# Performance work log

Hardware: AMD Instinct MI355X
Metric: run time of the kernel (lower is better)

The kernel has to match this reference:

```python
import jax, jax.numpy as jnp
import numpy as np

NUM_HEADS = 8
NUM_POINTS = 4


def setup_inputs() -> dict:
    key = jax.random.key(0)
    ks = jax.random.split(key, 10)
    B, H, W, D = 8, 64, 64, 256
    N = H * W
    nh, P = NUM_HEADS, NUM_POINTS

    def xavier(k, shape):
        fan_in, fan_out = shape[0], shape[1]
        lim = float(np.sqrt(6.0 / (fan_in + fan_out)))
        return jax.random.uniform(k, shape, jnp.float32, -lim, lim)

    x = jax.random.normal(ks[0], (B, N, D), jnp.float32)
    qkv_w = xavier(ks[1], (D, 3 * D))
    qkv_b = jnp.zeros((3 * D,), jnp.float32)
    # offset network is zero-init in the module; use small random weights so the
    # deformable sampling is actually exercised (offsets nonzero).
    off_w = jax.random.normal(ks[2], (D, nh * P * 2), jnp.float32) * 0.01
    off_b = jnp.zeros((nh * P * 2,), jnp.float32)
    attw_w = xavier(ks[3], (D, nh * P))
    attw_b = jnp.zeros((nh * P,), jnp.float32)
    proj_w = xavier(ks[4], (D, D))
    proj_b = jnp.zeros((D,), jnp.float32)
    return {
        "x": x, "qkv_w": qkv_w, "qkv_b": qkv_b,
        "off_w": off_w, "off_b": off_b,
        "attw_w": attw_w, "attw_b": attw_b,
        "proj_w": proj_w, "proj_b": proj_b,
        "H": 64, "W": 64,
    }


def _deformable_forward(x, qkv_w, qkv_b, off_w, off_b, attw_w, attw_b, proj_w, proj_b, H, W):
    B, N, D = x.shape
    nh, P = NUM_HEADS, NUM_POINTS
    hd = D // nh

    qkv = x @ qkv_w + qkv_b                      # [B,N,3D] (q,k computed but unused, as in the original)
    v = qkv[..., 2 * D:].reshape(B, N, nh, hd)   # [B,N,nh,hd]

    offsets = jnp.tanh((x @ off_w + off_b).reshape(B, N, nh, P, 2)) * 2.0

    ys, xs = jnp.meshgrid(jnp.arange(H, dtype=x.dtype), jnp.arange(W, dtype=x.dtype), indexing="ij")
    ref = jnp.stack([xs, ys], axis=-1).reshape(N, 2)          # [N,2] (x,y) pixel coords
    loc = ref[None, :, None, None, :] + offsets               # [B,N,nh,P,2] pixel coords
    # (module normalizes to [-1,1] then grid_sample align_corners=True un-normalizes
    #  back to exactly these pixel coordinates, so we sample at `loc` directly)

    # value as flat spatial map per head: [B,nh,hd,N], n = y*W + x
    vf = v.transpose(0, 2, 3, 1).reshape(B, nh, hd, N)

    gx, gy = loc[..., 0], loc[..., 1]
    x0 = jnp.floor(gx); y0 = jnp.floor(gy)
    x1 = x0 + 1.0;      y1 = y0 + 1.0
    wx1 = gx - x0; wx0 = 1.0 - wx1
    wy1 = gy - y0; wy0 = 1.0 - wy1

    def corner(xi, yi, w):
        # bilinear corner with zeros padding: zero weight if corner out of bounds
        valid = (xi >= 0) & (xi < W) & (yi >= 0) & (yi < H)
        idx = (jnp.clip(yi, 0, H - 1) * W + jnp.clip(xi, 0, W - 1)).astype(jnp.int32)
        idx2 = idx.transpose(0, 2, 1, 3).reshape(B, nh, N * P)          # [B,nh,N*P]
        g = jnp.take_along_axis(vf, idx2[:, :, None, :], axis=3)        # [B,nh,hd,N*P]
        w2 = (w * valid.astype(x.dtype)).transpose(0, 2, 1, 3).reshape(B, nh, 1, N * P)
        return g * w2

    sampled = (corner(x0, y0, wx0 * wy0) + corner(x1, y0, wx1 * wy0)
               + corner(x0, y1, wx0 * wy1) + corner(x1, y1, wx1 * wy1))
    sampled = sampled.reshape(B, nh, hd, N, P)

    attn = jax.nn.softmax((x @ attw_w + attw_b).reshape(B, N, nh, P), axis=-1)
    out = jnp.einsum("bhcnp,bnhp->bnhc", sampled, attn).reshape(B, N, D)
    return out @ proj_w + proj_b


def reference(x, qkv_w, qkv_b, off_w, off_b, attw_w, attw_b, proj_w, proj_b, H, W):
    return _deformable_forward(x, qkv_w, qkv_b, off_w, off_b, attw_w, attw_b, proj_w, proj_b, H, W)
```

## Files before the change

kernel.cpp:

```cpp
#include <hip/hip_runtime.h>
#include <hip/hip_bf16.h>
#include <cmath>

#define NN 4096
typedef __attribute__((ext_vector_type(8))) short short8;
typedef __attribute__((ext_vector_type(4))) float f32x4;

__device__ __forceinline__ float bf2f(unsigned short u) {
  union { unsigned int i; float f; } c; c.i = ((unsigned int)u) << 16; return c.f;
}

__global__ __launch_bounds__(256) void cvt_w(
    const float* __restrict__ qkv_w, const float* __restrict__ off_w,
    const float* __restrict__ attw_w, const float* __restrict__ proj_w,
    __hip_bfloat16* __restrict__ wcatT, __hip_bfloat16* __restrict__ pjT)
{
  const int t = threadIdx.x;
  if (blockIdx.x < 256) {
    int k = blockIdx.x;
    wcatT[t * 256 + k] = __float2bfloat16(qkv_w[k * 768 + 512 + t]);
    if (t < 128) {
      int c2 = 256 + t;
      float v = 0.f;
      if (c2 < 320)      v = off_w[k * 64 + (c2 - 256)];
      else if (c2 < 352) v = attw_w[k * 32 + (c2 - 320)];
      wcatT[c2 * 256 + k] = __float2bfloat16(v);
    }
  } else {
    int k = blockIdx.x - 256;
    pjT[t * 256 + k] = __float2bfloat16(proj_w[k * 256 + t]);
  }
}

__global__ __launch_bounds__(512) void gemm_voff(
    const float* __restrict__ x,
    const __hip_bfloat16* __restrict__ wcatT,
    const float* __restrict__ vbias,
    const float* __restrict__ off_b, const float* __restrict__ attw_b,
    __hip_bfloat16* __restrict__ vb,
    unsigned int* __restrict__ table)
{
  __shared__ float smemf[12800];
  short* As = (short*)smemf;
  short* Bs = As + 128 * 40;
  float (*L)[100] = (float(*)[100])smemf;

  const int t = threadIdx.x;
  const int m0 = blockIdx.x * 128;
  const int wave = t >> 6, lane = t & 63, q = lane >> 4, ln = lane & 15;
  const int wm = (wave & 1) * 64, wn = (wave >> 1) * 96;

  f32x4 acc[4][6] = {};

  const int arow = t >> 2, aseg = t & 3;
  const float* apg = x + (size_t)(m0 + arow) * 256 + aseg * 8;

  for (int k0 = 0; k0 < 256; k0 += 32) {
    float4 f0 = *(const float4*)(apg + k0);
    float4 f1 = *(const float4*)(apg + k0 + 4);
    alignas(16) __hip_bfloat16 cv[8] = {
      __float2bfloat16(f0.x), __float2bfloat16(f0.y), __float2bfloat16(f0.z), __float2bfloat16(f0.w),
      __float2bfloat16(f1.x), __float2bfloat16(f1.y), __float2bfloat16(f1.z), __float2bfloat16(f1.w)};
    *(int4*)&As[arow * 40 + aseg * 8] = *(int4*)cv;
#pragma unroll
    for (int i = 0; i < 3; ++i) {
      int u = t + i * 512;
      int brow = u >> 2, bseg = u & 3;
      *(int4*)&Bs[brow * 40 + bseg * 8] =
          *(const int4*)&wcatT[(size_t)brow * 256 + k0 + bseg * 8];
    }
    __syncthreads();
    short8 a[4], b[6];
#pragma unroll
    for (int i = 0; i < 4; ++i) a[i] = *(const short8*)&As[(wm + i * 16 + ln) * 40 + q * 8];
#pragma unroll
    for (int j = 0; j < 6; ++j) b[j] = *(const short8*)&Bs[(wn + j * 16 + ln) * 40 + q * 8];
#pragma unroll
    for (int i = 0; i < 4; ++i)
#pragma unroll
      for (int j = 0; j < 6; ++j)
        acc[i][j] = __builtin_amdgcn_mfma_f32_16x16x32_bf16(a[i], b[j], acc[i][j], 0, 0, 0);
    __syncthreads();
  }

#pragma unroll
  for (int j = 0; j < 6; ++j) {
    int col = wn + j * 16 + ln;
    if (col < 256) {
      float bv = vbias[col];
#pragma unroll
      for (int i = 0; i < 4; ++i) {
        int rowb = m0 + wm + i * 16 + q * 4;
#pragma unroll
        for (int r = 0; r < 4; ++r)
          vb[(size_t)(rowb + r) * 256 + col] = __float2bfloat16(acc[i][j][r] + bv);
      }
    } else if (col < 352) {
      int lc = col - 256;
      float bv = (lc < 64) ? off_b[lc] : attw_b[lc - 64];
#pragma unroll
      for (int i = 0; i < 4; ++i)
#pragma unroll
        for (int r = 0; r < 4; ++r)
          L[wm + i * 16 + q * 4 + r][lc] = acc[i][j][r] + bv;
    }
  }
  __syncthreads();

#pragma unroll
  for (int it = 0; it < 2; ++it) {
    int pl = t + it * 512;
    int rr = pl >> 3, h = pl & 7;
    int row = m0 + rr;
    int nl = row & (NN - 1);
    float refx = (float)(nl & 63);
    float refy = (float)(nl >> 6);

    float a0 = L[rr][64 + h * 4 + 0], a1 = L[rr][64 + h * 4 + 1];
    float a2 = L[rr][64 + h * 4 + 2], a3 = L[rr][64 + h * 4 + 3];
    float mx = fmaxf(fmaxf(a0, a1), fmaxf(a2, a3));
    float e0 = expf(a0 - mx), e1 = expf(a1 - mx), e2 = expf(a2 - mx), e3 = expf(a3 - mx);
    float inv = 1.f / (e0 + e1 + e2 + e3);
    float at[4] = {e0 * inv, e1 * inv, e2 * inv, e3 * inv};

    alignas(16) unsigned short idxs[16];
    alignas(16) _Float16 wsv[16];
#pragma unroll
    for (int p = 0; p < 4; ++p) {
      float gx = refx + 2.f * tanhf(L[rr][h * 8 + p * 2 + 0]);
      float gy = refy + 2.f * tanhf(L[rr][h * 8 + p * 2 + 1]);
      float x0f = floorf(gx), y0f = floorf(gy);
      int x0 = (int)x0f, y0 = (int)y0f;
      int x1 = x0 + 1,   y1 = y0 + 1;
      float wx1 = gx - x0f, wx0 = 1.f - wx1;
      float wy1 = gy - y0f, wy0 = 1.f - wy1;
      int cx0 = min(max(x0, 0), 63), cx1 = min(max(x1, 0), 63);
      int cy0 = min(max(y0, 0), 63), cy1 = min(max(y1, 0), 63);
      float vx0 = (x0 >= 0 && x0 <= 63) ? 1.f : 0.f;
      float vx1 = (x1 >= 0 && x1 <= 63) ? 1.f : 0.f;
      float vy0 = (y0 >= 0 && y0 <= 63) ? 1.f : 0.f;
      float vy1 = (y1 >= 0 && y1 <= 63) ? 1.f : 0.f;
      float ap = at[p];
      idxs[p * 4 + 0] = (unsigned short)(cy0 * 64 + cx0);
      idxs[p * 4 + 1] = (unsigned short)(cy0 * 64 + cx1);
      idxs[p * 4 + 2] = (unsigned short)(cy1 * 64 + cx0);
      idxs[p * 4 + 3] = (unsigned short)(cy1 * 64 + cx1);
      wsv[p * 4 + 0] = (_Float16)(ap * wx0 * wy0 * vx0 * vy0);
      wsv[p * 4 + 1] = (_Float16)(ap * wx1 * wy0 * vx1 * vy0);
      wsv[p * 4 + 2] = (_Float16)(ap * wx0 * wy1 * vx0 * vy1);
      wsv[p * 4 + 3] = (_Float16)(ap * wx1 * wy1 * vx1 * vy1);
    }
    uint4* dst = (uint4*)(table + ((size_t)row * 8 + h) * 16);
    dst[0] = *(uint4*)&idxs[0];
    dst[1] = *(uint4*)&idxs[8];
    dst[2] = *(uint4*)&wsv[0];
    dst[3] = *(uint4*)&wsv[8];
  }
}

__global__ __launch_bounds__(256) void sample_kernel(
    const __hip_bfloat16* __restrict__ v,
    const unsigned int* __restrict__ table,
    __hip_bfloat16* __restrict__ y)
{
  __shared__ uint4 Tab[256];
  const int t = threadIdx.x;
  const int p0 = blockIdx.x * 64;
  Tab[t] = *(const uint4*)(table + (size_t)p0 * 16 + t * 4);
  __syncthreads();

  const int g = t & 3, p = t >> 2;
  const int pg = p0 + p;
  const int h = pg & 7;
  const int row = pg >> 3;
  const int b = row >> 12;
  const unsigned short* ip = (const unsigned short*)&Tab[p * 4];
  const _Float16* wp = (const _Float16*)((const char*)&Tab[p * 4] + 32);
  const char* vbase = (const char*)(v + (size_t)b * NN * 256 + h * 32 + g * 8);

  float acc[8] = {};
#pragma unroll
  for (int j = 0; j < 16; ++j) {
    float w = (float)wp[j];
    int idx = ip[j];
    int4 pk = *(const int4*)(vbase + (size_t)idx * 512);
    const unsigned short* u = (const unsigned short*)&pk;
#pragma unroll
    for (int c = 0; c < 8; ++c) acc[c] += w * bf2f(u[c]);
  }
  alignas(16) __hip_bfloat16 o[8];
#pragma unroll
  for (int c = 0; c < 8; ++c) o[c] = __float2bfloat16(acc[c]);
  *(int4*)((char*)y + ((size_t)row * 256 + h * 32 + g * 8) * 2) = *(int4*)o;
}

__global__ __launch_bounds__(256) void gemm_proj(
    const short* __restrict__ A, const short* __restrict__ BT,
    const float* __restrict__ bias, float* __restrict__ out)
{
  __shared__ short As[128 * 40];
  __shared__ short Bs[128 * 40];
  const int t = threadIdx.x;
  const int m0 = blockIdx.y * 128, n0 = blockIdx.x * 128;
  const int wave = t >> 6, lane = t & 63, q = lane >> 4, ln = lane & 15;
  const int wm = (wave & 1) * 64, wn = (wave >> 1) * 64;

  f32x4 acc[4][4] = {};

  for (int k0 = 0; k0 < 256; k0 += 32) {
#pragma unroll
    for (int u = 0; u < 2; ++u) {
      int c = t + u * 256;
      int row = c >> 2, kq = c & 3;
      *(int4*)&As[row * 40 + kq * 8] =
          *(const int4*)&A[(size_t)(m0 + row) * 256 + k0 + kq * 8];
      *(int4*)&Bs[row * 40 + kq * 8] =
          *(const int4*)&BT[(size_t)(n0 + row) * 256 + k0 + kq * 8];
    }
    __syncthreads();
    short8 a[4], b[4];
#pragma unroll
    for (int i = 0; i < 4; ++i) a[i] = *(const short8*)&As[(wm + i * 16 + ln) * 40 + q * 8];
#pragma unroll
    for (int j = 0; j < 4; ++j) b[j] = *(const short8*)&Bs[(wn + j * 16 + ln) * 40 + q * 8];
#pragma unroll
    for (int i = 0; i < 4; ++i)
#pragma unroll
      for (int j = 0; j < 4; ++j)
        acc[i][j] = __builtin_amdgcn_mfma_f32_16x16x32_bf16(a[i], b[j], acc[i][j], 0, 0, 0);
    __syncthreads();
  }

#pragma unroll
  for (int j = 0; j < 4; ++j) {
    int col = n0 + wn + j * 16 + ln;
    float bv = bias[col];
#pragma unroll
    for (int i = 0; i < 4; ++i) {
      int rowb = m0 + wm + i * 16 + q * 4;
#pragma unroll
      for (int r = 0; r < 4; ++r)
        out[(size_t)(rowb + r) * 256 + col] = acc[i][j][r] + bv;
    }
  }
}

extern "C" void kernel_launch(void* const* d_in, const int* in_sizes, int n_in,
                              void* d_out, int out_size, void* d_ws, size_t ws_size,
                              hipStream_t stream) {
  const float* x      = (const float*)d_in[0];
  const float* qkv_w  = (const float*)d_in[1];
  const float* qkv_b  = (const float*)d_in[2];
  const float* off_w  = (const float*)d_in[3];
  const float* off_b  = (const float*)d_in[4];
  const float* attw_w = (const float*)d_in[5];
  const float* attw_b = (const float*)d_in[6];
  const float* proj_w = (const float*)d_in[7];
  const float* proj_b = (const float*)d_in[8];
  float* out = (float*)d_out;

  char* ws = (char*)d_ws;
  __hip_bfloat16* vb    = (__hip_bfloat16*)(ws);
  __hip_bfloat16* yb    = (__hip_bfloat16*)(ws + 16777216);
  unsigned int*   table = (unsigned int*)  (ws + 33554432);
  __hip_bfloat16* wcatT = (__hip_bfloat16*)(ws + 50331648);
  __hip_bfloat16* pjT   = (__hip_bfloat16*)(ws + 50528256);

  cvt_w<<<512, 256, 0, stream>>>(qkv_w, off_w, attw_w, proj_w, wcatT, pjT);
  gemm_voff<<<256, 512, 0, stream>>>(x, wcatT, qkv_b + 512, off_b, attw_b, vb, table);
  sample_kernel<<<4096, 256, 0, stream>>>(vb, table, yb);
  dim3 g2(2, 256);
  gemm_proj<<<g2, 256, 0, stream>>>((const short*)yb, (const short*)pjT, proj_b, out);
}
```

Baseline: 154.1 us.

## Fuse deformable sampling into projection GEMM and shrink voff tiles to 64 rows

The sampling kernel and the projection GEMM are merged: each block gathers and bilinearly blends 64 rows of sampled values straight into shared memory as the GEMM A operand, then multiplies by the full 256-column projection weight. This removes the intermediate bf16 buffer round trip through global memory and one launch. The value/offset GEMM now uses 64-row tiles with 256 threads and 512 blocks, and both kernels remap block indices so that consecutive blocks are spread across batches, changing L2 locality. In exchange the fused kernel uses more shared memory, which lowers occupancy, and the gather phase can no longer overlap with MFMA work inside a block.

```diff
diff --git a/kernel.cpp b/kernel.cpp
--- a/kernel.cpp
+++ b/kernel.cpp
@@ -32,7 +32,7 @@
   }
 }
 
-__global__ __launch_bounds__(512) void gemm_voff(
+__global__ __launch_bounds__(256) void gemm_voff(
     const float* __restrict__ x,
     const __hip_bfloat16* __restrict__ wcatT,
     const float* __restrict__ vbias,
@@ -40,15 +40,16 @@
     __hip_bfloat16* __restrict__ vb,
     unsigned int* __restrict__ table)
 {
-  __shared__ float smemf[12800];
+  __shared__ float smemf[8960];
   short* As = (short*)smemf;
-  short* Bs = As + 128 * 40;
+  short* Bs = As + 64 * 40;
   float (*L)[100] = (float(*)[100])smemf;
 
   const int t = threadIdx.x;
-  const int m0 = blockIdx.x * 128;
+  const int bid = blockIdx.x;
+  const int m0 = (((bid & 7) << 6) | (bid >> 3)) * 64;
   const int wave = t >> 6, lane = t & 63, q = lane >> 4, ln = lane & 15;
-  const int wm = (wave & 1) * 64, wn = (wave >> 1) * 96;
+  const int wn = wave * 96;
 
   f32x4 acc[4][6] = {};
 
@@ -63,8 +64,8 @@
       __float2bfloat16(f1.x), __float2bfloat16(f1.y), __float2bfloat16(f1.z), __float2bfloat16(f1.w)};
     *(int4*)&As[arow * 40 + aseg * 8] = *(int4*)cv;
 #pragma unroll
-    for (int i = 0; i < 3; ++i) {
-      int u = t + i * 512;
+    for (int i = 0; i < 6; ++i) {
+      int u = t + i * 256;
       int brow = u >> 2, bseg = u & 3;
       *(int4*)&Bs[brow * 40 + bseg * 8] =
           *(const int4*)&wcatT[(size_t)brow * 256 + k0 + bseg * 8];
@@ -72,7 +73,7 @@
     __syncthreads();
     short8 a[4], b[6];
 #pragma unroll
-    for (int i = 0; i < 4; ++i) a[i] = *(const short8*)&As[(wm + i * 16 + ln) * 40 + q * 8];
+    for (int i = 0; i < 4; ++i) a[i] = *(const short8*)&As[(i * 16 + ln) * 40 + q * 8];
 #pragma unroll
     for (int j = 0; j < 6; ++j) b[j] = *(const short8*)&Bs[(wn + j * 16 + ln) * 40 + q * 8];
 #pragma unroll
@@ -90,7 +91,7 @@
       float bv = vbias[col];
 #pragma unroll
       for (int i = 0; i < 4; ++i) {
-        int rowb = m0 + wm + i * 16 + q * 4;
+        int rowb = m0 + i * 16 + q * 4;
 #pragma unroll
         for (int r = 0; r < 4; ++r)
           vb[(size_t)(rowb + r) * 256 + col] = __float2bfloat16(acc[i][j][r] + bv);
@@ -102,14 +103,14 @@
       for (int i = 0; i < 4; ++i)
 #pragma unroll
         for (int r = 0; r < 4; ++r)
-          L[wm + i * 16 + q * 4 + r][lc] = acc[i][j][r] + bv;
+          L[i * 16 + q * 4 + r][lc] = acc[i][j][r] + bv;
     }
   }
   __syncthreads();
 
 #pragma unroll
   for (int it = 0; it < 2; ++it) {
-    int pl = t + it * 512;
+    int pl = t + it * 256;
     int rr = pl >> 3, h = pl & 7;
     int row = m0 + rr;
     int nl = row & (NN - 1);
@@ -158,69 +159,65 @@
   }
 }
 
-__global__ __launch_bounds__(256) void sample_kernel(
+__global__ __launch_bounds__(256) void sample_proj(
     const __hip_bfloat16* __restrict__ v,
     const unsigned int* __restrict__ table,
-    __hip_bfloat16* __restrict__ y)
+    const short* __restrict__ BT,
+    const float* __restrict__ bias,
+    float* __restrict__ out)
 {
-  __shared__ uint4 Tab[256];
+  __shared__ short As[64 * 264];
+  __shared__ short Bs[256 * 40];
   const int t = threadIdx.x;
-  const int p0 = blockIdx.x * 64;
-  Tab[t] = *(const uint4*)(table + (size_t)p0 * 16 + t * 4);
+  const int bid = blockIdx.x;
+  const int m0 = (((bid & 7) << 6) | (bid >> 3)) * 64;
+
+#pragma unroll 2
+  for (int it = 0; it < 8; ++it) {
+    int task = t + it * 256;
+    int g = task & 3, pairL = task >> 2;
+    int h = pairL & 7, rr = pairL >> 3;
+    int row = m0 + rr;
+    size_t pg = (size_t)row * 8 + h;
+    const uint4* te = (const uint4*)(table + pg * 16);
+    alignas(16) uint4 tb[4];
+    tb[0] = te[0]; tb[1] = te[1]; tb[2] = te[2]; tb[3] = te[3];
+    const unsigned short* ip = (const unsigned short*)tb;
+    const _Float16* wp = (const _Float16*)(tb + 2);
+    const char* vbase = (const char*)(v + (size_t)(row >> 12) * NN * 256 + h * 32 + g * 8);
+    float sacc[8] = {};
+#pragma unroll
+    for (int j = 0; j < 16; ++j) {
+      float w = (float)wp[j];
+      int idx = ip[j];
+      int4 pk = *(const int4*)(vbase + (size_t)idx * 512);
+      const unsigned short* u = (const unsigned short*)&pk;
+#pragma unroll
+      for (int c = 0; c < 8; ++c) sacc[c] += w * bf2f(u[c]);
+    }
+    alignas(16) __hip_bfloat16 o[8];
+#pragma unroll
+    for (int c = 0; c < 8; ++c) o[c] = __float2bfloat16(sacc[c]);
+    *(int4*)&As[rr * 264 + h * 32 + g * 8] = *(int4*)o;
+  }
   __syncthreads();
 
-  const int g = t & 3, p = t >> 2;
-  const int pg = p0 + p;
-  const int h = pg & 7;
-  const int row = pg >> 3;
-  const int b = row >> 12;
-  const unsigned short* ip = (const unsigned short*)&Tab[p * 4];
-  const _Float16* wp = (const _Float16*)((const char*)&Tab[p * 4] + 32);
-  const char* vbase = (const char*)(v + (size_t)b * NN * 256 + h * 32 + g * 8);
-
-  float acc[8] = {};
-#pragma unroll
-  for (int j = 0; j < 16; ++j) {
-    float w = (float)wp[j];
-    int idx = ip[j];
-    int4 pk = *(const int4*)(vbase + (size_t)idx * 512);
-    const unsigned short* u = (const unsigned short*)&pk;
-#pragma unroll
-    for (int c = 0; c < 8; ++c) acc[c] += w * bf2f(u[c]);
-  }
-  alignas(16) __hip_bfloat16 o[8];
-#pragma unroll
-  for (int c = 0; c < 8; ++c) o[c] = __float2bfloat16(acc[c]);
-  *(int4*)((char*)y + ((size_t)row * 256 + h * 32 + g * 8) * 2) = *(int4*)o;
-}
-
-__global__ __launch_bounds__(256) void gemm_proj(
-    const short* __restrict__ A, const short* __restrict__ BT,
-    const float* __restrict__ bias, float* __restrict__ out)
-{
-  __shared__ short As[128 * 40];
-  __shared__ short Bs[128 * 40];
-  const int t = threadIdx.x;
-  const int m0 = blockIdx.y * 128, n0 = blockIdx.x * 128;
   const int wave = t >> 6, lane = t & 63, q = lane >> 4, ln = lane & 15;
-  const int wm = (wave & 1) * 64, wn = (wave >> 1) * 64;
-
+  const int wn = wave * 64;
   f32x4 acc[4][4] = {};
 
   for (int k0 = 0; k0 < 256; k0 += 32) {
 #pragma unroll
-    for (int u = 0; u < 2; ++u) {
-      int c = t + u * 256;
-      int row = c >> 2, kq = c & 3;
-      *(int4*)&As[row * 40 + kq * 8] =
-          *(const int4*)&A[(size_t)(m0 + row) * 256 + k0 + kq * 8];
-      *(int4*)&Bs[row * 40 + kq * 8] =
-          *(const int4*)&BT[(size_t)(n0 + row) * 256 + k0 + kq * 8];
+    for (int u2 = 0; u2 < 4; ++u2) {
+      int c = t + u2 * 256;
+      int col = c >> 2, kq = c & 3;
+      *(int4*)&Bs[col * 40 + kq * 8] =
+          *(const int4*)&BT[(size_t)col * 256 + k0 + kq * 8];
     }
     __syncthreads();
     short8 a[4], b[4];
 #pragma unroll
-    for (int i = 0; i < 4; ++i) a[i] = *(const short8*)&As[(wm + i * 16 + ln) * 40 + q * 8];
+    for (int i = 0; i < 4; ++i) a[i] = *(const short8*)&As[(i * 16 + ln) * 264 + k0 + q * 8];
 #pragma unroll
     for (int j = 0; j < 4; ++j) b[j] = *(const short8*)&Bs[(wn + j * 16 + ln) * 40 + q * 8];
 #pragma unroll
@@ -233,11 +230,11 @@
 
 #pragma unroll
   for (int j = 0; j < 4; ++j) {
-    int col = n0 + wn + j * 16 + ln;
+    int col = wn + j * 16 + ln;
     float bv = bias[col];
 #pragma unroll
     for (int i = 0; i < 4; ++i) {
-      int rowb = m0 + wm + i * 16 + q * 4;
+      int rowb = m0 + i * 16 + q * 4;
 #pragma unroll
       for (int r = 0; r < 4; ++r)
         out[(size_t)(rowb + r) * 256 + col] = acc[i][j][r] + bv;
@@ -261,14 +258,11 @@
 
   char* ws = (char*)d_ws;
   __hip_bfloat16* vb    = (__hip_bfloat16*)(ws);
-  __hip_bfloat16* yb    = (__hip_bfloat16*)(ws + 16777216);
-  unsigned int*   table = (unsigned int*)  (ws + 33554432);
-  __hip_bfloat16* wcatT = (__hip_bfloat16*)(ws + 50331648);
-  __hip_bfloat16* pjT   = (__hip_bfloat16*)(ws + 50528256);
+  unsigned int*   table = (unsigned int*)  (ws + 16777216);
+  __hip_bfloat16* wcatT = (__hip_bfloat16*)(ws + 33554432);
+  __hip_bfloat16* pjT   = (__hip_bfloat16*)(ws + 33751040);
 
   cvt_w<<<512, 256, 0, stream>>>(qkv_w, off_w, attw_w, proj_w, wcatT, pjT);
-  gemm_voff<<<256, 512, 0, stream>>>(x, wcatT, qkv_b + 512, off_b, attw_b, vb, table);
-  sample_kernel<<<4096, 256, 0, stream>>>(vb, table, yb);
-  dim3 g2(2, 256);
-  gemm_proj<<<g2, 256, 0, stream>>>((const short*)yb, (const short*)pjT, proj_b, out);
-}
+  gemm_voff<<<512, 256, 0, stream>>>(x, wcatT, qkv_b + 512, off_b, attw_b, vb, table);
+  sample_proj<<<512, 256, 0, stream>>>(vb, table, (const short*)pjT, proj_b, out);
+}
```

Measured after the change: 182.7 us. +18.6%, slower.
